# Kernel optimization log

Measured on AMD Instinct MI355X. Metric: run time of the kernel, lower is better.

Reference implementation:

```python
import jax, jax.numpy as jnp
import numpy as np

B, C, N, K = 2, 64, 65536, 16
OUT = 64


def setup_inputs() -> dict:
    key = jax.random.key(0)
    k1, k2, k3, k4 = jax.random.split(key, 4)
    x = jax.random.normal(k1, (B, C, N, 1), dtype=jnp.float32)
    edge_index = jax.random.randint(k2, (2, B, N, K), 0, N, dtype=jnp.int64)
    # 1x1 conv weight of MLP2dLayer([2*C, OUT]) and its bias
    W = jax.random.normal(k3, (OUT, 2 * C), dtype=jnp.float32) * (1.0 / np.sqrt(2 * C))
    b = jax.random.normal(k4, (OUT,), dtype=jnp.float32) * 0.01
    return {"x": x, "edge_index": edge_index, "W": W, "b": b}


def reference(x, edge_index, W, b):
    # x: [B, C, N, 1], edge_index: [2, B, N, K]
    Bs, Cs, Ns, _ = x.shape
    Ks = edge_index.shape[-1]
    feat = x[..., 0]                                   # [B, C, N]
    idx = edge_index[0].reshape(Bs, 1, Ns * Ks)        # [B, 1, N*K]
    idx = jnp.broadcast_to(idx, (Bs, Cs, Ns * Ks))
    x_j = jnp.take_along_axis(feat, idx, axis=2).reshape(Bs, Cs, Ns, Ks)  # gather neighbors
    x_i = jnp.broadcast_to(x[..., :1], (Bs, Cs, Ns, Ks))                  # repeated center feature
    msg = jnp.concatenate([x_i, x_j - x_i], axis=1)    # [B, 2C, N, K]
    h = jnp.einsum("oi,bink->bonk", W, msg) + b[None, :, None, None]
    h = jax.nn.relu(h)                                 # MLP2dLayer: 1x1 conv + relu (norm=None)
    out = jnp.max(h, axis=-1, keepdims=True)           # max aggregation over neighbors
    return out
```

## Files before the change

### kernel.cpp

```cpp
#include <hip/hip_runtime.h>


using u32 = unsigned int;
using u16 = unsigned short;
using u8 = unsigned char;
typedef short short8 __attribute__((ext_vector_type(8)));
typedef float f32x4 __attribute__((ext_vector_type(4)));
typedef int i32x4 __attribute__((ext_vector_type(4)));
typedef u32 u32x4 __attribute__((ext_vector_type(4)));

#define NN 65536
#define VSCL 15.875f
#define VDEQ 0.0629921260f

static __device__ __forceinline__ u16 bf16r(float a) {
  u32 u = __builtin_bit_cast(u32, a);
  return (u16)((u + 0x7fffu + ((u >> 16) & 1u)) >> 16);
}
static __device__ __forceinline__ u32 pack_bf16(float a, float b) {
  return (u32)bf16r(a) | ((u32)bf16r(b) << 16);
}
static __device__ __forceinline__ float bflo(u32 x) {
  return __builtin_bit_cast(float, x << 16);
}
static __device__ __forceinline__ float bfhi(u32 x) {
  return __builtin_bit_cast(float, x & 0xffff0000u);
}

__global__ __launch_bounds__(256) void prep_w(const float* __restrict__ W,
                                              u32* __restrict__ Wcat) {
  int id = blockIdx.x * 256 + threadIdx.x;
  int o = id >> 5, c2 = id & 31;
  float f0, f1;
  if (o < 64) {
    f0 = W[o * 128 + 2 * c2]     - W[o * 128 + 64 + 2 * c2];
    f1 = W[o * 128 + 2 * c2 + 1] - W[o * 128 + 64 + 2 * c2 + 1];
  } else {
    int om = o - 64;
    f0 = W[om * 128 + 64 + 2 * c2];
    f1 = W[om * 128 + 64 + 2 * c2 + 1];
  }
  Wcat[id] = pack_bf16(f0, f1);
}

__global__ __launch_bounds__(256, 6) void k1(const float* __restrict__ x,
                                             const float* __restrict__ bias,
                                             const u32* __restrict__ Wcat,
                                             u32* __restrict__ Up,
                                             u32* __restrict__ V8p) {
  __shared__ __align__(16) char smem[26880];
  u32* Wb = (u32*)smem;
  u32* Xa = (u32*)(smem + 18432);

  int t = threadIdx.x;
  int l = t & 63;
  int w = t >> 6;
  int b = blockIdx.x >> 10;
  int n0 = (blockIdx.x & 1023) << 6;

#pragma unroll
  for (int i = 0; i < 16; ++i) {
    int id = i * 256 + t;
    Wb[(id >> 5) * 36 + (id & 31)] = Wcat[id];
  }
#pragma unroll
  for (int r = 0; r < 8; ++r) {
    int c2 = r * 4 + w;
    size_t base = ((size_t)(b * 64 + 2 * c2)) * NN + n0 + l;
    Xa[l * 33 + c2] = pack_bf16(x[base], x[base + NN]);
  }
  __syncthreads();

  f32x4 acc[8];
#pragma unroll
  for (int f = 0; f < 8; ++f) acc[f] = {0.f, 0.f, 0.f, 0.f};

#pragma unroll
  for (int kb = 0; kb < 2; ++kb) {
    int ar = (16 * w + (l & 15)) * 33 + kb * 16 + 4 * (l >> 4);
    i32x4 av = {(int)Xa[ar], (int)Xa[ar + 1], (int)Xa[ar + 2], (int)Xa[ar + 3]};
    short8 a = __builtin_bit_cast(short8, av);
#pragma unroll
    for (int f = 0; f < 8; ++f) {
      i32x4 bv = *(const i32x4*)(Wb + (16 * f + (l & 15)) * 36 + kb * 16 + 4 * (l >> 4));
      short8 bb = __builtin_bit_cast(short8, bv);
      acc[f] = __builtin_amdgcn_mfma_f32_16x16x32_bf16(a, bb, acc[f], 0, 0, 0);
    }
  }

  float bs[4];
#pragma unroll
  for (int f = 0; f < 4; ++f) bs[f] = bias[16 * f + (l & 15)];

  __syncthreads();
  u16* TRU16 = (u16*)smem;
  u8* TRV8 = (u8*)(smem + 8448);
#pragma unroll
  for (int f = 0; f < 4; ++f) {
#pragma unroll
    for (int r = 0; r < 4; ++r) {
      int node = 16 * w + 4 * (l >> 4) + r;
      int o = 16 * f + (l & 15);
      float uval = acc[f][r] + bs[f];
      float vval = acc[f + 4][r];
      TRU16[node * 66 + o] = bf16r(uval);
      float q = fminf(fmaxf(vval * VSCL, -127.f), 127.f);
      TRV8[node * 68 + o] = (u8)((int)rintf(q) + 128);
    }
  }
  __syncthreads();

  u32* TRU32 = (u32*)smem;
  u32* TRV32 = (u32*)(smem + 8448);
#pragma unroll
  for (int i = 0; i < 8; ++i) {
    int id = i * 256 + t;
    int node = id >> 5, c = id & 31;
    Up[((size_t)b * NN + n0 + node) * 32 + c] = TRU32[node * 33 + c];
  }
#pragma unroll
  for (int i = 0; i < 4; ++i) {
    int id = i * 256 + t;
    int node = id >> 4, c = id & 15;
    V8p[((size_t)b * NN + n0 + node) * 16 + c] = TRV32[node * 17 + c];
  }
}

__global__ __launch_bounds__(256, 6) void k2(const int* __restrict__ eidx,
                                             const u32* __restrict__ Up,
                                             const u32* __restrict__ V8p,
                                             float* __restrict__ out) {
  __shared__ __align__(16) int eixT[16 * 65];
  __shared__ __align__(16) float tile[64 * 65];

  int t = threadIdx.x;
  int bx = blockIdx.x;
  int slot = bx & 7;
  int b = slot & 1;
  int quad = slot >> 1;
  int n0 = (((bx >> 3) + (quad << 8))) << 6;

  {
    i32x4 v = __builtin_nontemporal_load(
        (const i32x4*)(eidx + ((size_t)b * NN + n0) * 16) + t);
    int node = t >> 2, e0 = (t & 3) * 4;
    eixT[(e0 + 0) * 65 + node] = v.x;
    eixT[(e0 + 1) * 65 + node] = v.y;
    eixT[(e0 + 2) * 65 + node] = v.z;
    eixT[(e0 + 3) * 65 + node] = v.w;
  }
  __syncthreads();

  int l = t & 63, w = t >> 6;
  int node = w * 16 + (l >> 2);
  int qq = l & 3;

  const u32* Vb = V8p + ((size_t)b * NN) * 16 + qq * 4;
  float mx[16];
#pragma unroll
  for (int i = 0; i < 16; ++i) mx[i] = 0.f;

#pragma unroll
  for (int hb = 0; hb < 4; ++hb) {
    u32x4 vr[4];
#pragma unroll
    for (int e = 0; e < 4; ++e) {
      int id = eixT[(hb * 4 + e) * 65 + node];
      vr[e] = *(const u32x4*)(Vb + (size_t)id * 16);
    }
#pragma unroll
    for (int e = 0; e < 4; ++e) {
#pragma unroll
      for (int d = 0; d < 4; ++d) {
        u32 dw = vr[e][d];
        mx[4 * d + 0] = fmaxf(mx[4 * d + 0], (float)(dw & 0xffu));
        mx[4 * d + 1] = fmaxf(mx[4 * d + 1], (float)((dw >> 8) & 0xffu));
        mx[4 * d + 2] = fmaxf(mx[4 * d + 2], (float)((dw >> 16) & 0xffu));
        mx[4 * d + 3] = fmaxf(mx[4 * d + 3], (float)((dw >> 24) & 0xffu));
      }
    }
  }

  size_t ub = ((size_t)b * NN + n0 + node) * 32 + qq * 8;
  u32x4 uv0 = __builtin_nontemporal_load((const u32x4*)(Up + ub));
  u32x4 uv1 = __builtin_nontemporal_load((const u32x4*)(Up + ub + 4));
#pragma unroll
  for (int cc = 0; cc < 8; ++cc) {
    u32 uw = cc < 4 ? uv0[cc] : uv1[cc - 4];
    int o = qq * 16 + 2 * cc;
    tile[o * 65 + node] =
        fmaxf(bflo(uw) + (mx[2 * cc] - 128.f) * VDEQ, 0.f);
    tile[(o + 1) * 65 + node] =
        fmaxf(bfhi(uw) + (mx[2 * cc + 1] - 128.f) * VDEQ, 0.f);
  }
  __syncthreads();

#pragma unroll
  for (int r = 0; r < 16; ++r) {
    int o = r * 4 + w;
    __builtin_nontemporal_store(
        tile[o * 65 + l],
        out + ((size_t)(b * 64 + o)) * NN + n0 + l);
  }
}

extern "C" void kernel_launch(void* const* d_in, const int* in_sizes, int n_in,
                              void* d_out, int out_size, void* d_ws, size_t ws_size,
                              hipStream_t stream) {
  const float* x = (const float*)d_in[0];
  const int* eidx = (const int*)d_in[1];
  const float* W = (const float*)d_in[2];
  const float* bias = (const float*)d_in[3];

  u32* Up = (u32*)d_ws;
  u32* V8p = Up + (size_t)2 * NN * 32;
  u32* Wcat = (u32*)((char*)d_ws + (size_t)24 * 1024 * 1024);

  prep_w<<<16, 256, 0, stream>>>(W, Wcat);
  k1<<<2 * 1024, 256, 0, stream>>>(x, bias, Wcat, Up, V8p);
  k2<<<2 * 1024, 256, 0, stream>>>(eidx, Up, V8p, (float*)d_out);
}
```

Baseline: 50.56 us.

## Remap k2 threads to 8 nodes x 8 channel groups, store output directly

Reworks the k2 gather kernel so each thread handles 8 output channels for one node across two passes, with 8 consecutive nodes per channel group in a wavefront. Writes now go straight to global memory instead of through the transposed LDS tile, which drops the tile buffer and a barrier. The launch-bounds occupancy hint rises from 6 to 8. The cost is that each store instruction writes only 8 contiguous floats (32 bytes) per channel row, so stores are less coalesced than the old 64-float rows, and the gather loads shrink to 8 bytes per lane.

```diff
diff --git a/kernel.cpp b/kernel.cpp
--- a/kernel.cpp
+++ b/kernel.cpp
@@ -8,6 +8,7 @@
 typedef float f32x4 __attribute__((ext_vector_type(4)));
 typedef int i32x4 __attribute__((ext_vector_type(4)));
 typedef u32 u32x4 __attribute__((ext_vector_type(4)));
+typedef u32 u32x2 __attribute__((ext_vector_type(2)));
 
 #define NN 65536
 #define VSCL 15.875f
@@ -126,19 +127,18 @@
   }
 }
 
-__global__ __launch_bounds__(256, 6) void k2(const int* __restrict__ eidx,
+__global__ __launch_bounds__(256, 8) void k2(const int* __restrict__ eidx,
                                              const u32* __restrict__ Up,
                                              const u32* __restrict__ V8p,
                                              float* __restrict__ out) {
   __shared__ __align__(16) int eixT[16 * 65];
-  __shared__ __align__(16) float tile[64 * 65];
 
   int t = threadIdx.x;
   int bx = blockIdx.x;
   int slot = bx & 7;
   int b = slot & 1;
   int quad = slot >> 1;
-  int n0 = (((bx >> 3) + (quad << 8))) << 6;
+  int n0 = ((bx >> 3) + (quad << 8)) << 6;
 
   {
     i32x4 v = __builtin_nontemporal_load(
@@ -152,55 +152,53 @@
   __syncthreads();
 
   int l = t & 63, w = t >> 6;
-  int node = w * 16 + (l >> 2);
-  int qq = l & 3;
-
-  const u32* Vb = V8p + ((size_t)b * NN) * 16 + qq * 4;
-  float mx[16];
-#pragma unroll
-  for (int i = 0; i < 16; ++i) mx[i] = 0.f;
-
-#pragma unroll
-  for (int hb = 0; hb < 4; ++hb) {
-    u32x4 vr[4];
-#pragma unroll
-    for (int e = 0; e < 4; ++e) {
-      int id = eixT[(hb * 4 + e) * 65 + node];
-      vr[e] = *(const u32x4*)(Vb + (size_t)id * 16);
-    }
-#pragma unroll
-    for (int e = 0; e < 4; ++e) {
-#pragma unroll
-      for (int d = 0; d < 4; ++d) {
-        u32 dw = vr[e][d];
-        mx[4 * d + 0] = fmaxf(mx[4 * d + 0], (float)(dw & 0xffu));
-        mx[4 * d + 1] = fmaxf(mx[4 * d + 1], (float)((dw >> 8) & 0xffu));
-        mx[4 * d + 2] = fmaxf(mx[4 * d + 2], (float)((dw >> 16) & 0xffu));
-        mx[4 * d + 3] = fmaxf(mx[4 * d + 3], (float)((dw >> 24) & 0xffu));
+  int ns = l & 7;
+  int c8 = l >> 3;
+
+  const u32* Vb = V8p + ((size_t)b * NN) * 16 + c8 * 2;
+
+#pragma unroll
+  for (int pass = 0; pass < 2; ++pass) {
+    int node = w * 16 + pass * 8 + ns;
+
+    float mx[8];
+#pragma unroll
+    for (int i = 0; i < 8; ++i) mx[i] = 0.f;
+
+#pragma unroll
+    for (int hb = 0; hb < 4; ++hb) {
+      u32x2 vr[4];
+#pragma unroll
+      for (int e = 0; e < 4; ++e) {
+        int id = eixT[(hb * 4 + e) * 65 + node];
+        vr[e] = *(const u32x2*)(Vb + (size_t)id * 16);
       }
-    }
-  }
-
-  size_t ub = ((size_t)b * NN + n0 + node) * 32 + qq * 8;
-  u32x4 uv0 = __builtin_nontemporal_load((const u32x4*)(Up + ub));
-  u32x4 uv1 = __builtin_nontemporal_load((const u32x4*)(Up + ub + 4));
-#pragma unroll
-  for (int cc = 0; cc < 8; ++cc) {
-    u32 uw = cc < 4 ? uv0[cc] : uv1[cc - 4];
-    int o = qq * 16 + 2 * cc;
-    tile[o * 65 + node] =
-        fmaxf(bflo(uw) + (mx[2 * cc] - 128.f) * VDEQ, 0.f);
-    tile[(o + 1) * 65 + node] =
-        fmaxf(bfhi(uw) + (mx[2 * cc + 1] - 128.f) * VDEQ, 0.f);
-  }
-  __syncthreads();
-
-#pragma unroll
-  for (int r = 0; r < 16; ++r) {
-    int o = r * 4 + w;
-    __builtin_nontemporal_store(
-        tile[o * 65 + l],
-        out + ((size_t)(b * 64 + o)) * NN + n0 + l);
+#pragma unroll
+      for (int e = 0; e < 4; ++e) {
+#pragma unroll
+        for (int d = 0; d < 2; ++d) {
+          u32 dw = vr[e][d];
+          mx[4 * d + 0] = fmaxf(mx[4 * d + 0], (float)(dw & 0xffu));
+          mx[4 * d + 1] = fmaxf(mx[4 * d + 1], (float)((dw >> 8) & 0xffu));
+          mx[4 * d + 2] = fmaxf(mx[4 * d + 2], (float)((dw >> 16) & 0xffu));
+          mx[4 * d + 3] = fmaxf(mx[4 * d + 3], (float)((dw >> 24) & 0xffu));
+        }
+      }
+    }
+
+    u32x4 uv = __builtin_nontemporal_load(
+        (const u32x4*)(Up + ((size_t)b * NN + n0 + node) * 32 + c8 * 4));
+    float* ob = out + ((size_t)(b * 64 + c8 * 8)) * NN + n0 + node;
+#pragma unroll
+    for (int j = 0; j < 4; ++j) {
+      u32 uw = uv[j];
+      __builtin_nontemporal_store(
+          fmaxf(bflo(uw) + (mx[2 * j] - 128.f) * VDEQ, 0.f),
+          ob + (size_t)(2 * j) * NN);
+      __builtin_nontemporal_store(
+          fmaxf(bfhi(uw) + (mx[2 * j + 1] - 128.f) * VDEQ, 0.f),
+          ob + (size_t)(2 * j + 1) * NN);
+    }
   }
 }
 
```

After: 70.19 us. 38.8% more time.
